# Kernel optimization log

Hardware: AMD Instinct MI355X
Metric: run time of the kernel (lower is better)

Reference implementation:

```python
import jax, jax.numpy as jnp
import numpy as np

NHEADS = 16

def setup_inputs() -> dict:
    key = jax.random.key(0)
    ks = jax.random.split(key, 11)
    B, S, D = 2, 2048, 1024
    std = 1.0 / np.sqrt(D)
    return {
        "query": jax.random.normal(ks[0], (B, S, D), jnp.float32),
        "key":   jax.random.normal(ks[1], (B, S, D), jnp.float32),
        "value": jax.random.normal(ks[2], (B, S, D), jnp.float32),
        "Wq": jax.random.normal(ks[3], (D, D), jnp.float32) * std,
        "bq": jax.random.normal(ks[4], (D,), jnp.float32) * std,
        "Wk": jax.random.normal(ks[5], (D, D), jnp.float32) * std,
        "bk": jax.random.normal(ks[6], (D,), jnp.float32) * std,
        "Wv": jax.random.normal(ks[7], (D, D), jnp.float32) * std,
        "bv": jax.random.normal(ks[8], (D,), jnp.float32) * std,
        "Wo": jax.random.normal(ks[9], (D, D), jnp.float32) * std,
        "bo": jax.random.normal(ks[10], (D,), jnp.float32) * std,
    }

def reference(query, key, value, Wq, bq, Wk, bk, Wv, bv, Wo, bo):
    B, Sq, D = query.shape
    Sk = key.shape[1]
    H = NHEADS
    hd = D // H
    q = (query @ Wq + bq).reshape(B, Sq, H, hd)
    k = (key @ Wk + bk).reshape(B, Sk, H, hd)
    v = (value @ Wv + bv).reshape(B, Sk, H, hd)
    # Explicit [B,H,Sq,Sk] score tensor, as in the original
    score = jnp.einsum('bqhd,bkhd->bhqk', q, k)
    # masked=True: causal mask applied before scaling (equivalent: -inf/c = -inf)
    cmask = jnp.triu(jnp.ones((Sq, Sk), dtype=bool), k=1)
    score = jnp.where(cmask, -jnp.inf, score)
    # NOTE: original divides by sqrt(score.shape[-1]) == sqrt(Sk), NOT sqrt(head_dim)
    scale = jnp.float32(1.0 / np.sqrt(Sk))
    att = jax.nn.softmax(score * scale, axis=-1)
    ret = jnp.einsum('bhqk,bkhd->bqhd', att, v).reshape(B, Sq, D)
    return ret @ Wo + bo
```

## Files before the change

### kernel.cpp

```cpp
#include <hip/hip_runtime.h>
#include <stdint.h>

typedef unsigned short u16;
typedef unsigned int u32;
typedef __bf16 bf16x8 __attribute__((ext_vector_type(8)));
typedef __bf16 bf16x4 __attribute__((ext_vector_type(4)));
typedef float f32x4 __attribute__((ext_vector_type(4)));

__device__ __forceinline__ u16 f2bf(float f) {
  u32 u = __float_as_uint(f);
  u = (u + 0x7fffu + ((u >> 16) & 1u)) >> 16;
  return (u16)u;
}

__device__ __forceinline__ void gload16(const void* g, void* l) {
  __builtin_amdgcn_global_load_lds(
      (const __attribute__((address_space(1))) void*)g,
      (__attribute__((address_space(3))) void*)l, 16, 0, 0);
}

__global__ __launch_bounds__(256) void prep_k(
    const float* __restrict__ q, const float* __restrict__ k,
    const float* __restrict__ v, u16* __restrict__ dst,
    const float* __restrict__ w0, const float* __restrict__ w1,
    const float* __restrict__ w2, const float* __restrict__ w3,
    u16* __restrict__ wt) {
  const int id = blockIdx.x;
  if (id < 6144) {
    const int y = id >> 11;
    const int x = id & 2047;
    const float* s = (y == 0) ? q : (y == 1) ? k : v;
    u16* d = dst + (size_t)y * 4194304u;
    int e = (x * 256 + threadIdx.x) * 8;
    float4 a = *(const float4*)(s + e);
    float4 b = *(const float4*)(s + e + 4);
    uint4 o;
    o.x = (u32)f2bf(a.x) | ((u32)f2bf(a.y) << 16);
    o.y = (u32)f2bf(a.z) | ((u32)f2bf(a.w) << 16);
    o.z = (u32)f2bf(b.x) | ((u32)f2bf(b.y) << 16);
    o.w = (u32)f2bf(b.z) | ((u32)f2bf(b.w) << 16);
    *(uint4*)(d + e) = o;
    return;
  }
  __shared__ float tile[64][65];
  const int t = id - 6144;
  const int z = t >> 8;
  const int rem = t & 255;
  const int x0 = (rem & 15) * 64, y0 = (rem >> 4) * 64;
  const float* W = (z == 0) ? w0 : (z == 1) ? w1 : (z == 2) ? w2 : w3;
  u16* Wt = wt + (size_t)z * 1048576u;
  const int tx = threadIdx.x & 63, ty = threadIdx.x >> 6;
#pragma unroll
  for (int j = 0; j < 16; ++j)
    tile[ty + j * 4][tx] = W[(size_t)(y0 + ty + j * 4) * 1024 + x0 + tx];
  __syncthreads();
#pragma unroll
  for (int j = 0; j < 16; ++j)
    Wt[(size_t)(x0 + ty + j * 4) * 1024 + y0 + tx] = f2bf(tile[tx][ty + j * 4]);
}

__global__ __launch_bounds__(256, 3) void gemm_proj(
    const u16* __restrict__ Xb, const u16* __restrict__ Wt,
    const float* __restrict__ bqp, const float* __restrict__ bkp,
    const float* __restrict__ bvp,
    u16* __restrict__ Qb, u16* __restrict__ Kb, u16* __restrict__ VtG,
    float qsc) {
  const int z = blockIdx.z;
  const u16 *A, *Bt;
  const float* bias;
  u16* C;
  int N, bm, bn;
  float osc = 1.f;
  bool rowb = false;
  if (z < 2) {
    A = Xb + (size_t)z * 4194304u;
    Bt = Wt + (size_t)z * 1048576u;
    bias = z ? bkp : bqp;
    C = z ? Kb : Qb;
    N = 1024;
    bm = blockIdx.x * 128;
    bn = blockIdx.y * 128;
    if (z == 0) osc = qsc;
  } else {
    A = Wt + 2u * 1048576u;
    Bt = Xb + 2u * 4194304u;
    bias = bvp;
    C = VtG;
    N = 4096;
    bm = blockIdx.y * 128;
    bn = blockIdx.x * 128;
    rowb = true;
  }

  __shared__ __align__(16) u16 ldsA[128 * 64];
  __shared__ __align__(16) u16 ldsB[128 * 64];

  const int tid = threadIdx.x;
  const int lane = tid & 63, wv = tid >> 6;
  const int wr = wv >> 1, wc = wv & 1;
  const int l15 = lane & 15, l4 = lane >> 4;

  const f32x4 zero4 = {0.f, 0.f, 0.f, 0.f};
  f32x4 acc[4][4];
#pragma unroll
  for (int i = 0; i < 4; ++i)
#pragma unroll
    for (int j = 0; j < 4; ++j) acc[i][j] = zero4;

  for (int kt = 0; kt < 16; ++kt) {
    __syncthreads();
#pragma unroll
    for (int g = 0; g < 4; ++g) {
      int p = g * 256 + tid;
      int row = p >> 3;
      int ss = (p & 7) ^ (row & 7);
      gload16(A + (size_t)(bm + row) * 1024 + kt * 64 + ss * 8,
              (char*)ldsA + (g * 256 + wv * 64) * 16);
    }
#pragma unroll
    for (int g = 0; g < 4; ++g) {
      int p = g * 256 + tid;
      int row = p >> 3;
      int ss = (p & 7) ^ (row & 7);
      gload16(Bt + (size_t)(bn + row) * 1024 + kt * 64 + ss * 8,
              (char*)ldsB + (g * 256 + wv * 64) * 16);
    }
    __syncthreads();

    bf16x8 af[4][2], bfr[4][2];
#pragma unroll
    for (int mf = 0; mf < 4; ++mf) {
      int row = wr * 64 + mf * 16 + l15;
#pragma unroll
      for (int ks = 0; ks < 2; ++ks) {
        int byt = row * 128 + ((ks * 64 + l4 * 16) ^ ((row & 7) << 4));
        af[mf][ks] = *(const bf16x8*)((const char*)ldsA + byt);
      }
    }
#pragma unroll
    for (int nf = 0; nf < 4; ++nf) {
      int row = wc * 64 + nf * 16 + l15;
#pragma unroll
      for (int ks = 0; ks < 2; ++ks) {
        int byt = row * 128 + ((ks * 64 + l4 * 16) ^ ((row & 7) << 4));
        bfr[nf][ks] = *(const bf16x8*)((const char*)ldsB + byt);
      }
    }
#pragma unroll
    for (int mf = 0; mf < 4; ++mf)
#pragma unroll
      for (int nf = 0; nf < 4; ++nf) {
        acc[mf][nf] = __builtin_amdgcn_mfma_f32_16x16x32_bf16(
            af[mf][0], bfr[nf][0], acc[mf][nf], 0, 0, 0);
        acc[mf][nf] = __builtin_amdgcn_mfma_f32_16x16x32_bf16(
            af[mf][1], bfr[nf][1], acc[mf][nf], 0, 0, 0);
      }
  }

  float bcol[4];
  if (!rowb) {
#pragma unroll
    for (int nf = 0; nf < 4; ++nf)
      bcol[nf] = bias[bn + wc * 64 + nf * 16 + l15];
  }
#pragma unroll
  for (int mf = 0; mf < 4; ++mf) {
#pragma unroll
    for (int i = 0; i < 4; ++i) {
      int r = bm + wr * 64 + mf * 16 + l4 * 4 + i;
      float br = rowb ? bias[r] : 0.f;
#pragma unroll
      for (int nf = 0; nf < 4; ++nf) {
        int c = bn + wc * 64 + nf * 16 + l15;
        float val = (acc[mf][nf][i] + (rowb ? br : bcol[nf])) * osc;
        C[(size_t)r * N + c] = f2bf(val);
      }
    }
  }
}

__global__ __launch_bounds__(256, 3) void gemm_out(
    const u16* __restrict__ A, const u16* __restrict__ Bt,
    const float* __restrict__ bias, float* __restrict__ C) {
  __shared__ __align__(16) u16 ldsA[128 * 64];
  __shared__ __align__(16) u16 ldsB[128 * 64];

  const int tid = threadIdx.x;
  const int lane = tid & 63, wv = tid >> 6;
  const int wr = wv >> 1, wc = wv & 1;
  const int l15 = lane & 15, l4 = lane >> 4;
  const int bm = blockIdx.x * 128, bn = blockIdx.y * 128;

  const f32x4 zero4 = {0.f, 0.f, 0.f, 0.f};
  f32x4 acc[4][4];
#pragma unroll
  for (int i = 0; i < 4; ++i)
#pragma unroll
    for (int j = 0; j < 4; ++j) acc[i][j] = zero4;

  for (int kt = 0; kt < 16; ++kt) {
    __syncthreads();
#pragma unroll
    for (int g = 0; g < 4; ++g) {
      int p = g * 256 + tid;
      int row = p >> 3;
      int ss = (p & 7) ^ (row & 7);
      gload16(A + (size_t)(bm + row) * 1024 + kt * 64 + ss * 8,
              (char*)ldsA + (g * 256 + wv * 64) * 16);
    }
#pragma unroll
    for (int g = 0; g < 4; ++g) {
      int p = g * 256 + tid;
      int row = p >> 3;
      int ss = (p & 7) ^ (row & 7);
      gload16(Bt + (size_t)(bn + row) * 1024 + kt * 64 + ss * 8,
              (char*)ldsB + (g * 256 + wv * 64) * 16);
    }
    __syncthreads();

    bf16x8 af[4][2], bfr[4][2];
#pragma unroll
    for (int mf = 0; mf < 4; ++mf) {
      int row = wr * 64 + mf * 16 + l15;
#pragma unroll
      for (int ks = 0; ks < 2; ++ks) {
        int byt = row * 128 + ((ks * 64 + l4 * 16) ^ ((row & 7) << 4));
        af[mf][ks] = *(const bf16x8*)((const char*)ldsA + byt);
      }
    }
#pragma unroll
    for (int nf = 0; nf < 4; ++nf) {
      int row = wc * 64 + nf * 16 + l15;
#pragma unroll
      for (int ks = 0; ks < 2; ++ks) {
        int byt = row * 128 + ((ks * 64 + l4 * 16) ^ ((row & 7) << 4));
        bfr[nf][ks] = *(const bf16x8*)((const char*)ldsB + byt);
      }
    }
#pragma unroll
    for (int mf = 0; mf < 4; ++mf)
#pragma unroll
      for (int nf = 0; nf < 4; ++nf) {
        acc[mf][nf] = __builtin_amdgcn_mfma_f32_16x16x32_bf16(
            af[mf][0], bfr[nf][0], acc[mf][nf], 0, 0, 0);
        acc[mf][nf] = __builtin_amdgcn_mfma_f32_16x16x32_bf16(
            af[mf][1], bfr[nf][1], acc[mf][nf], 0, 0, 0);
      }
  }

  float bcol[4];
#pragma unroll
  for (int nf = 0; nf < 4; ++nf)
    bcol[nf] = bias[bn + wc * 64 + nf * 16 + l15];
#pragma unroll
  for (int mf = 0; mf < 4; ++mf) {
#pragma unroll
    for (int i = 0; i < 4; ++i) {
      int r = bm + wr * 64 + mf * 16 + l4 * 4 + i;
#pragma unroll
      for (int nf = 0; nf < 4; ++nf) {
        int c = bn + wc * 64 + nf * 16 + l15;
        C[(size_t)r * 1024 + c] = acc[mf][nf][i] + bcol[nf];
      }
    }
  }
}

__global__ __launch_bounds__(256, 2) void attn_k(
    const u16* __restrict__ Q, const u16* __restrict__ Kb,
    const u16* __restrict__ Vt, u16* __restrict__ ctx) {
  const int id = blockIdx.x + (blockIdx.y << 4);
  const int xcd = id & 7;
  const int kk = id >> 3;
  const int bh = xcd * 4 + (kk & 3);
  const int qtA = kk >> 2;
  const int qtB = 31 - qtA;
  const int b = bh >> 4, h = bh & 15;
  const int tid = threadIdx.x;
  const int lane = tid & 63, wv = tid >> 6;
  const int l15 = lane & 15, l4 = lane >> 4;

  __shared__ __align__(16) u16 Kt[2][64 * 64];
  __shared__ __align__(16) u16 Vl[2][64 * 64];
  __shared__ __align__(16) u16 Pl[4][16 * 64];

  const u16* KB = Kb + (size_t)(b * 2048) * 1024 + h * 64;
  const u16* VB = Vt + (size_t)(h * 64) * 4096 + b * 2048;

  const u16* qpa =
      Q + (size_t)(b * 2048 + qtA * 64 + wv * 16 + l15) * 1024 + h * 64;
  const u16* qpb =
      Q + (size_t)(b * 2048 + qtB * 64 + wv * 16 + l15) * 1024 + h * 64;
  bf16x8 qa0 = *(const bf16x8*)(qpa + l4 * 8);
  bf16x8 qa1 = *(const bf16x8*)(qpa + 32 + l4 * 8);
  bf16x8 qb0 = *(const bf16x8*)(qpb + l4 * 8);
  bf16x8 qb1 = *(const bf16x8*)(qpb + 32 + l4 * 8);

  const f32x4 zero4 = {0.f, 0.f, 0.f, 0.f};
  f32x4 oA[4], oB[4];
#pragma unroll
  for (int i = 0; i < 4; ++i) { oA[i] = zero4; oB[i] = zero4; }
  float mA = -1e30f, lsA = 0.f, mB = -1e30f, lsB = 0.f;

  auto issueKV = [&](int jt, int bufi) {
    const u16* kb = KB + (size_t)(jt * 64) * 1024;
#pragma unroll
    for (int g = 0; g < 2; ++g) {
      int p = g * 256 + tid;
      int row = p >> 3;
      int ss = (p & 7) ^ (row & 7);
      gload16(kb + (size_t)row * 1024 + ss * 8,
              (char*)(&Kt[bufi][0]) + (g * 256 + wv * 64) * 16);
    }
#pragma unroll
    for (int g = 0; g < 2; ++g) {
      int p = g * 256 + tid;
      int d = p >> 3;
      int ss = (p & 7) ^ (d & 7);
      gload16(VB + (size_t)d * 4096 + jt * 64 + ss * 8,
              (char*)(&Vl[bufi][0]) + (g * 256 + wv * 64) * 16);
    }
  };

  auto computeTile = [&](int cur, bool diag, bf16x8 qf0, bf16x8 qf1,
                         float& m, float& lsum, f32x4* oacc) {
    f32x4 p4[4];
    __builtin_amdgcn_s_setprio(1);
#pragma unroll
    for (int nt = 0; nt < 4; ++nt) {
      int row = nt * 16 + l15;
      int sw = (row & 7) << 4;
      const char* kr = (const char*)&Kt[cur][0] + row * 128;
      bf16x8 k0 = *(const bf16x8*)(kr + ((l4 * 16) ^ sw));
      bf16x8 k1 = *(const bf16x8*)(kr + ((64 + l4 * 16) ^ sw));
      f32x4 s = zero4;
      s = __builtin_amdgcn_mfma_f32_16x16x32_bf16(k0, qf0, s, 0, 0, 0);
      s = __builtin_amdgcn_mfma_f32_16x16x32_bf16(k1, qf1, s, 0, 0, 0);
      p4[nt] = s;
    }
    __builtin_amdgcn_s_setprio(0);

    if (diag) {
#pragma unroll
      for (int nt = 0; nt < 4; ++nt)
#pragma unroll
        for (int i = 0; i < 4; ++i)
          if (nt * 16 + l4 * 4 + i > wv * 16 + l15) p4[nt][i] = -1e30f;
    }

    float rm = p4[0][0];
#pragma unroll
    for (int nt = 0; nt < 4; ++nt)
#pragma unroll
      for (int i = 0; i < 4; ++i) rm = fmaxf(rm, p4[nt][i]);
    rm = fmaxf(rm, __shfl_xor(rm, 16, 64));
    rm = fmaxf(rm, __shfl_xor(rm, 32, 64));

    if (!__all(rm - m <= 8.0f)) {
      float mn = fmaxf(m, rm);
      float ce = exp2f(m - mn);
      m = mn;
      lsum *= ce;
#pragma unroll
      for (int i = 0; i < 4; ++i) {
        float cei = __shfl(ce, (lane & 48) | (l4 * 4 + i), 64);
#pragma unroll
        for (int nt = 0; nt < 4; ++nt) oacc[nt][i] *= cei;
      }
    }

    float rs = 0.f;
#pragma unroll
    for (int nt = 0; nt < 4; ++nt)
#pragma unroll
      for (int i = 0; i < 4; ++i) {
        float e = exp2f(p4[nt][i] - m);
        p4[nt][i] = e;
        rs += e;
      }
    rs += __shfl_xor(rs, 16, 64);
    rs += __shfl_xor(rs, 32, 64);
    lsum += rs;

    {
      int sw = (l15 & 7) << 4;
#pragma unroll
      for (int nt = 0; nt < 4; ++nt) {
        bf16x4 pb = __builtin_convertvector(p4[nt], bf16x4);
        *(bf16x4*)((char*)&Pl[wv][0] + l15 * 128 + ((nt * 32 + l4 * 8) ^ sw)) = pb;
      }
    }

    bf16x8 pa0, pa1;
    {
      int sw = (l15 & 7) << 4;
      pa0 = *(const bf16x8*)((const char*)&Pl[wv][0] + l15 * 128 + ((l4 * 16) ^ sw));
      pa1 = *(const bf16x8*)((const char*)&Pl[wv][0] + l15 * 128 +
                             ((64 + l4 * 16) ^ sw));
    }
    __builtin_amdgcn_s_setprio(1);
#pragma unroll
    for (int nt = 0; nt < 4; ++nt) {
      int d = nt * 16 + l15;
      int sw = (d & 7) << 4;
      const char* vr = (const char*)&Vl[cur][0] + d * 128;
      bf16x8 v0 = *(const bf16x8*)(vr + ((l4 * 16) ^ sw));
      bf16x8 v1 = *(const bf16x8*)(vr + ((64 + l4 * 16) ^ sw));
      oacc[nt] = __builtin_amdgcn_mfma_f32_16x16x32_bf16(pa0, v0, oacc[nt], 0, 0, 0);
      oacc[nt] = __builtin_amdgcn_mfma_f32_16x16x32_bf16(pa1, v1, oacc[nt], 0, 0, 0);
    }
    __builtin_amdgcn_s_setprio(0);
  };

  issueKV(0, 0);
  for (int j = 0; j <= qtB; ++j) {
    const int cur = j & 1;
    __syncthreads();
    if (j < qtB) issueKV(j + 1, cur ^ 1);
    computeTile(cur, j == qtB, qb0, qb1, mB, lsB, oB);
    if (j <= qtA) computeTile(cur, j == qtA, qa0, qa1, mA, lsA, oA);
  }

  float rcpA = 1.f / lsA;
  float rcpB = 1.f / lsB;
  u16* ca = ctx + (size_t)(b * 2048 + qtA * 64 + wv * 16) * 1024 + h * 64;
  u16* cb = ctx + (size_t)(b * 2048 + qtB * 64 + wv * 16) * 1024 + h * 64;
#pragma unroll
  for (int i = 0; i < 4; ++i) {
    int src = (lane & 48) | (l4 * 4 + i);
    float ivA = __shfl(rcpA, src, 64);
    float ivB = __shfl(rcpB, src, 64);
    int r = l4 * 4 + i;
#pragma unroll
    for (int nt = 0; nt < 4; ++nt) {
      ca[(size_t)r * 1024 + nt * 16 + l15] = f2bf(oA[nt][i] * ivA);
      cb[(size_t)r * 1024 + nt * 16 + l15] = f2bf(oB[nt][i] * ivB);
    }
  }
}

extern "C" void kernel_launch(void* const* d_in, const int* in_sizes, int n_in,
                              void* d_out, int out_size, void* d_ws,
                              size_t ws_size, hipStream_t stream) {
  const float* q  = (const float*)d_in[0];
  const float* k  = (const float*)d_in[1];
  const float* v  = (const float*)d_in[2];
  const float* Wq = (const float*)d_in[3];
  const float* bq = (const float*)d_in[4];
  const float* Wk = (const float*)d_in[5];
  const float* bk = (const float*)d_in[6];
  const float* Wv = (const float*)d_in[7];
  const float* bv = (const float*)d_in[8];
  const float* Wo = (const float*)d_in[9];
  const float* bo = (const float*)d_in[10];

  char* ws = (char*)d_ws;
  u16* Xb  = (u16*)ws;
  u16* Wt  = (u16*)(ws + 25165824);
  u16* VtG = (u16*)(ws + 33554432);
  u16* ctx = Xb;
  u16* Qb  = (u16*)d_out;
  u16* Kb  = Qb + 4194304;

  const float SC2A = 0.0318793585f;

  prep_k<<<dim3(7168), 256, 0, stream>>>(q, k, v, Xb, Wq, Wk, Wv, Wo, Wt);
  gemm_proj<<<dim3(32, 8, 3), 256, 0, stream>>>(Xb, Wt, bq, bk, bv, Qb, Kb,
                                                VtG, SC2A);
  attn_k<<<dim3(16, 32), 256, 0, stream>>>(Qb, Kb, VtG, ctx);
  gemm_out<<<dim3(32, 8), 256, 0, stream>>>(ctx, Wt + 3 * 1048576, bo,
                                            (float*)d_out);
}
```

Measured before the change: 114.4 us.

## Fuse fp32-to-bf16 activation conversion into projection GEMM staging

Removes the separate pass that converts q/k/v activations to bf16. The projection GEMM now reads fp32 activations directly, converts them in registers and writes them into LDS, while weights still use async global-to-LDS loads. This saves the write and re-read of a 24MB bf16 intermediate. In exchange, each GEMM tile reads fp32 data (twice the bytes, re-read across N tiles) through registers instead of direct LDS loads, and the MFMA block is also given a raised scheduling priority.

```diff
diff --git a/kernel.cpp b/kernel.cpp
--- a/kernel.cpp
+++ b/kernel.cpp
@@ -20,30 +20,11 @@
 }
 
 __global__ __launch_bounds__(256) void prep_k(
-    const float* __restrict__ q, const float* __restrict__ k,
-    const float* __restrict__ v, u16* __restrict__ dst,
     const float* __restrict__ w0, const float* __restrict__ w1,
     const float* __restrict__ w2, const float* __restrict__ w3,
     u16* __restrict__ wt) {
-  const int id = blockIdx.x;
-  if (id < 6144) {
-    const int y = id >> 11;
-    const int x = id & 2047;
-    const float* s = (y == 0) ? q : (y == 1) ? k : v;
-    u16* d = dst + (size_t)y * 4194304u;
-    int e = (x * 256 + threadIdx.x) * 8;
-    float4 a = *(const float4*)(s + e);
-    float4 b = *(const float4*)(s + e + 4);
-    uint4 o;
-    o.x = (u32)f2bf(a.x) | ((u32)f2bf(a.y) << 16);
-    o.y = (u32)f2bf(a.z) | ((u32)f2bf(a.w) << 16);
-    o.z = (u32)f2bf(b.x) | ((u32)f2bf(b.y) << 16);
-    o.w = (u32)f2bf(b.z) | ((u32)f2bf(b.w) << 16);
-    *(uint4*)(d + e) = o;
-    return;
-  }
   __shared__ float tile[64][65];
-  const int t = id - 6144;
+  const int t = blockIdx.x;
   const int z = t >> 8;
   const int rem = t & 255;
   const int x0 = (rem & 15) * 64, y0 = (rem >> 4) * 64;
@@ -60,21 +41,23 @@
 }
 
 __global__ __launch_bounds__(256, 3) void gemm_proj(
-    const u16* __restrict__ Xb, const u16* __restrict__ Wt,
+    const float* __restrict__ qin, const float* __restrict__ kin,
+    const float* __restrict__ vin, const u16* __restrict__ Wt,
     const float* __restrict__ bqp, const float* __restrict__ bkp,
     const float* __restrict__ bvp,
     u16* __restrict__ Qb, u16* __restrict__ Kb, u16* __restrict__ VtG,
     float qsc) {
   const int z = blockIdx.z;
-  const u16 *A, *Bt;
+  const float* Xf;
+  const u16* Wb;
   const float* bias;
   u16* C;
   int N, bm, bn;
   float osc = 1.f;
   bool rowb = false;
   if (z < 2) {
-    A = Xb + (size_t)z * 4194304u;
-    Bt = Wt + (size_t)z * 1048576u;
+    Xf = z ? kin : qin;
+    Wb = Wt + (size_t)z * 1048576u;
     bias = z ? bkp : bqp;
     C = z ? Kb : Qb;
     N = 1024;
@@ -82,8 +65,8 @@
     bn = blockIdx.y * 128;
     if (z == 0) osc = qsc;
   } else {
-    A = Wt + 2u * 1048576u;
-    Bt = Xb + 2u * 4194304u;
+    Wb = Wt + 2u * 1048576u;
+    Xf = vin;
     bias = bvp;
     C = VtG;
     N = 4096;
@@ -107,23 +90,42 @@
 #pragma unroll
     for (int j = 0; j < 4; ++j) acc[i][j] = zero4;
 
+  auto stageF32 = [&](const float* S, int baseRow, int kt, u16* lds) {
+#pragma unroll
+    for (int g = 0; g < 4; ++g) {
+      int p = g * 256 + tid;
+      int row = p >> 3;
+      int ss = (p & 7) ^ (row & 7);
+      const float* src = S + (size_t)(baseRow + row) * 1024 + kt * 64 + ss * 8;
+      float4 a = *(const float4*)(src);
+      float4 b = *(const float4*)(src + 4);
+      uint4 o;
+      o.x = (u32)f2bf(a.x) | ((u32)f2bf(a.y) << 16);
+      o.y = (u32)f2bf(a.z) | ((u32)f2bf(a.w) << 16);
+      o.z = (u32)f2bf(b.x) | ((u32)f2bf(b.y) << 16);
+      o.w = (u32)f2bf(b.z) | ((u32)f2bf(b.w) << 16);
+      *(uint4*)((char*)lds + (size_t)(g * 256 + tid) * 16) = o;
+    }
+  };
+  auto stageBf = [&](const u16* S, int baseRow, int kt, u16* lds) {
+#pragma unroll
+    for (int g = 0; g < 4; ++g) {
+      int p = g * 256 + tid;
+      int row = p >> 3;
+      int ss = (p & 7) ^ (row & 7);
+      gload16(S + (size_t)(baseRow + row) * 1024 + kt * 64 + ss * 8,
+              (char*)lds + (size_t)(g * 256 + wv * 64) * 16);
+    }
+  };
+
   for (int kt = 0; kt < 16; ++kt) {
     __syncthreads();
-#pragma unroll
-    for (int g = 0; g < 4; ++g) {
-      int p = g * 256 + tid;
-      int row = p >> 3;
-      int ss = (p & 7) ^ (row & 7);
-      gload16(A + (size_t)(bm + row) * 1024 + kt * 64 + ss * 8,
-              (char*)ldsA + (g * 256 + wv * 64) * 16);
-    }
-#pragma unroll
-    for (int g = 0; g < 4; ++g) {
-      int p = g * 256 + tid;
-      int row = p >> 3;
-      int ss = (p & 7) ^ (row & 7);
-      gload16(Bt + (size_t)(bn + row) * 1024 + kt * 64 + ss * 8,
-              (char*)ldsB + (g * 256 + wv * 64) * 16);
+    if (z < 2) {
+      stageF32(Xf, bm, kt, ldsA);
+      stageBf(Wb, bn, kt, ldsB);
+    } else {
+      stageBf(Wb, bm, kt, ldsA);
+      stageF32(Xf, bn, kt, ldsB);
     }
     __syncthreads();
 
@@ -146,6 +148,7 @@
         bfr[nf][ks] = *(const bf16x8*)((const char*)ldsB + byt);
       }
     }
+    __builtin_amdgcn_s_setprio(1);
 #pragma unroll
     for (int mf = 0; mf < 4; ++mf)
 #pragma unroll
@@ -155,6 +158,7 @@
         acc[mf][nf] = __builtin_amdgcn_mfma_f32_16x16x32_bf16(
             af[mf][1], bfr[nf][1], acc[mf][nf], 0, 0, 0);
       }
+    __builtin_amdgcn_s_setprio(0);
   }
 
   float bcol[4];
@@ -455,18 +459,17 @@
   const float* bo = (const float*)d_in[10];
 
   char* ws = (char*)d_ws;
-  u16* Xb  = (u16*)ws;
+  u16* ctx = (u16*)ws;
   u16* Wt  = (u16*)(ws + 25165824);
   u16* VtG = (u16*)(ws + 33554432);
-  u16* ctx = Xb;
   u16* Qb  = (u16*)d_out;
   u16* Kb  = Qb + 4194304;
 
   const float SC2A = 0.0318793585f;
 
-  prep_k<<<dim3(7168), 256, 0, stream>>>(q, k, v, Xb, Wq, Wk, Wv, Wo, Wt);
-  gemm_proj<<<dim3(32, 8, 3), 256, 0, stream>>>(Xb, Wt, bq, bk, bv, Qb, Kb,
-                                                VtG, SC2A);
+  prep_k<<<dim3(1024), 256, 0, stream>>>(Wq, Wk, Wv, Wo, Wt);
+  gemm_proj<<<dim3(32, 8, 3), 256, 0, stream>>>(q, k, v, Wt, bq, bk, bv,
+                                                Qb, Kb, VtG, SC2A);
   attn_k<<<dim3(16, 32), 256, 0, stream>>>(Qb, Kb, VtG, ctx);
   gemm_out<<<dim3(32, 8), 256, 0, stream>>>(ctx, Wt + 3 * 1048576, bo,
                                             (float*)d_out);
```

New measurement: 132.0 us. 15.4% more time.

## Fuse paired query tiles into one pass sharing K/V fragment loads

Applied to the files above, without the earlier changes.

While both query tiles A and B are active, the loop computes their scores and PV products together. Each K and V fragment is read from LDS once and used for both tiles, and the independent MFMA chains are interleaved to hide latency. When A is on its diagonal tile, B still needs the full tile, so B is left unmasked, which matches the old behaviour. The P scratch buffer doubles in size to hold both tiles, and register pressure rises, which may hurt the occupancy of 2 blocks per CU.

```diff
diff --git a/kernel.cpp b/kernel.cpp
--- a/kernel.cpp
+++ b/kernel.cpp
@@ -282,7 +282,7 @@
 
   __shared__ __align__(16) u16 Kt[2][64 * 64];
   __shared__ __align__(16) u16 Vl[2][64 * 64];
-  __shared__ __align__(16) u16 Pl[4][16 * 64];
+  __shared__ __align__(16) u16 Pl[4][32 * 64];
 
   const u16* KB = Kb + (size_t)(b * 2048) * 1024 + h * 64;
   const u16* VB = Vt + (size_t)(h * 64) * 4096 + b * 2048;
@@ -320,6 +320,40 @@
       gload16(VB + (size_t)d * 4096 + jt * 64 + ss * 8,
               (char*)(&Vl[bufi][0]) + (g * 256 + wv * 64) * 16);
     }
+  };
+
+  auto softmaxUpd = [&](f32x4* p4, float& m, float& ls, f32x4* oacc) {
+    float rm = p4[0][0];
+#pragma unroll
+    for (int nt = 0; nt < 4; ++nt)
+#pragma unroll
+      for (int i = 0; i < 4; ++i) rm = fmaxf(rm, p4[nt][i]);
+    rm = fmaxf(rm, __shfl_xor(rm, 16, 64));
+    rm = fmaxf(rm, __shfl_xor(rm, 32, 64));
+    if (!__all(rm - m <= 8.0f)) {
+      float mn = fmaxf(m, rm);
+      float ce = exp2f(m - mn);
+      m = mn;
+      ls *= ce;
+#pragma unroll
+      for (int i = 0; i < 4; ++i) {
+        float cei = __shfl(ce, (lane & 48) | (l4 * 4 + i), 64);
+#pragma unroll
+        for (int nt = 0; nt < 4; ++nt) oacc[nt][i] *= cei;
+      }
+    }
+    float rs = 0.f;
+#pragma unroll
+    for (int nt = 0; nt < 4; ++nt)
+#pragma unroll
+      for (int i = 0; i < 4; ++i) {
+        float e = exp2f(p4[nt][i] - m);
+        p4[nt][i] = e;
+        rs += e;
+      }
+    rs += __shfl_xor(rs, 16, 64);
+    rs += __shfl_xor(rs, 32, 64);
+    ls += rs;
   };
 
   auto computeTile = [&](int cur, bool diag, bf16x8 qf0, bf16x8 qf1,
@@ -339,7 +373,6 @@
       p4[nt] = s;
     }
     __builtin_amdgcn_s_setprio(0);
-
     if (diag) {
 #pragma unroll
       for (int nt = 0; nt < 4; ++nt)
@@ -347,65 +380,25 @@
         for (int i = 0; i < 4; ++i)
           if (nt * 16 + l4 * 4 + i > wv * 16 + l15) p4[nt][i] = -1e30f;
     }
-
-    float rm = p4[0][0];
-#pragma unroll
-    for (int nt = 0; nt < 4; ++nt)
-#pragma unroll
-      for (int i = 0; i < 4; ++i) rm = fmaxf(rm, p4[nt][i]);
-    rm = fmaxf(rm, __shfl_xor(rm, 16, 64));
-    rm = fmaxf(rm, __shfl_xor(rm, 32, 64));
-
-    if (!__all(rm - m <= 8.0f)) {
-      float mn = fmaxf(m, rm);
-      float ce = exp2f(m - mn);
-      m = mn;
-      lsum *= ce;
-#pragma unroll
-      for (int i = 0; i < 4; ++i) {
-        float cei = __shfl(ce, (lane & 48) | (l4 * 4 + i), 64);
-#pragma unroll
-        for (int nt = 0; nt < 4; ++nt) oacc[nt][i] *= cei;
-      }
-    }
-
-    float rs = 0.f;
-#pragma unroll
-    for (int nt = 0; nt < 4; ++nt)
-#pragma unroll
-      for (int i = 0; i < 4; ++i) {
-        float e = exp2f(p4[nt][i] - m);
-        p4[nt][i] = e;
-        rs += e;
-      }
-    rs += __shfl_xor(rs, 16, 64);
-    rs += __shfl_xor(rs, 32, 64);
-    lsum += rs;
-
-    {
-      int sw = (l15 & 7) << 4;
-#pragma unroll
-      for (int nt = 0; nt < 4; ++nt) {
-        bf16x4 pb = __builtin_convertvector(p4[nt], bf16x4);
-        *(bf16x4*)((char*)&Pl[wv][0] + l15 * 128 + ((nt * 32 + l4 * 8) ^ sw)) = pb;
-      }
-    }
-
-    bf16x8 pa0, pa1;
-    {
-      int sw = (l15 & 7) << 4;
-      pa0 = *(const bf16x8*)((const char*)&Pl[wv][0] + l15 * 128 + ((l4 * 16) ^ sw));
-      pa1 = *(const bf16x8*)((const char*)&Pl[wv][0] + l15 * 128 +
-                             ((64 + l4 * 16) ^ sw));
-    }
+    softmaxUpd(p4, m, lsum, oacc);
+    const int sw = (l15 & 7) << 4;
+#pragma unroll
+    for (int nt = 0; nt < 4; ++nt) {
+      bf16x4 pb = __builtin_convertvector(p4[nt], bf16x4);
+      *(bf16x4*)((char*)&Pl[wv][0] + l15 * 128 + ((nt * 32 + l4 * 8) ^ sw)) = pb;
+    }
+    bf16x8 pa0 =
+        *(const bf16x8*)((const char*)&Pl[wv][0] + l15 * 128 + ((l4 * 16) ^ sw));
+    bf16x8 pa1 = *(const bf16x8*)((const char*)&Pl[wv][0] + l15 * 128 +
+                                  ((64 + l4 * 16) ^ sw));
     __builtin_amdgcn_s_setprio(1);
 #pragma unroll
     for (int nt = 0; nt < 4; ++nt) {
       int d = nt * 16 + l15;
-      int sw = (d & 7) << 4;
+      int sw2 = (d & 7) << 4;
       const char* vr = (const char*)&Vl[cur][0] + d * 128;
-      bf16x8 v0 = *(const bf16x8*)(vr + ((l4 * 16) ^ sw));
-      bf16x8 v1 = *(const bf16x8*)(vr + ((64 + l4 * 16) ^ sw));
+      bf16x8 v0 = *(const bf16x8*)(vr + ((l4 * 16) ^ sw2));
+      bf16x8 v1 = *(const bf16x8*)(vr + ((64 + l4 * 16) ^ sw2));
       oacc[nt] = __builtin_amdgcn_mfma_f32_16x16x32_bf16(pa0, v0, oacc[nt], 0, 0, 0);
       oacc[nt] = __builtin_amdgcn_mfma_f32_16x16x32_bf16(pa1, v1, oacc[nt], 0, 0, 0);
     }
@@ -417,8 +410,69 @@
     const int cur = j & 1;
     __syncthreads();
     if (j < qtB) issueKV(j + 1, cur ^ 1);
-    computeTile(cur, j == qtB, qb0, qb1, mB, lsB, oB);
-    if (j <= qtA) computeTile(cur, j == qtA, qa0, qa1, mA, lsA, oA);
+
+    if (j <= qtA) {
+      f32x4 pA[4], pB[4];
+      __builtin_amdgcn_s_setprio(1);
+#pragma unroll
+      for (int nt = 0; nt < 4; ++nt) {
+        int row = nt * 16 + l15;
+        int sw = (row & 7) << 4;
+        const char* kr = (const char*)&Kt[cur][0] + row * 128;
+        bf16x8 k0 = *(const bf16x8*)(kr + ((l4 * 16) ^ sw));
+        bf16x8 k1 = *(const bf16x8*)(kr + ((64 + l4 * 16) ^ sw));
+        f32x4 sA = __builtin_amdgcn_mfma_f32_16x16x32_bf16(k0, qa0, zero4, 0, 0, 0);
+        f32x4 sB = __builtin_amdgcn_mfma_f32_16x16x32_bf16(k0, qb0, zero4, 0, 0, 0);
+        sA = __builtin_amdgcn_mfma_f32_16x16x32_bf16(k1, qa1, sA, 0, 0, 0);
+        sB = __builtin_amdgcn_mfma_f32_16x16x32_bf16(k1, qb1, sB, 0, 0, 0);
+        pA[nt] = sA;
+        pB[nt] = sB;
+      }
+      __builtin_amdgcn_s_setprio(0);
+
+      if (j == qtA) {
+#pragma unroll
+        for (int nt = 0; nt < 4; ++nt)
+#pragma unroll
+          for (int i = 0; i < 4; ++i)
+            if (nt * 16 + l4 * 4 + i > wv * 16 + l15) pA[nt][i] = -1e30f;
+      }
+
+      softmaxUpd(pA, mA, lsA, oA);
+      softmaxUpd(pB, mB, lsB, oB);
+
+      const int sw = (l15 & 7) << 4;
+      char* prA = (char*)&Pl[wv][0] + l15 * 128;
+      char* prB = (char*)&Pl[wv][0] + (16 + l15) * 128;
+#pragma unroll
+      for (int nt = 0; nt < 4; ++nt) {
+        *(bf16x4*)(prA + ((nt * 32 + l4 * 8) ^ sw)) =
+            __builtin_convertvector(pA[nt], bf16x4);
+        *(bf16x4*)(prB + ((nt * 32 + l4 * 8) ^ sw)) =
+            __builtin_convertvector(pB[nt], bf16x4);
+      }
+      bf16x8 paA0 = *(const bf16x8*)(prA + ((l4 * 16) ^ sw));
+      bf16x8 paA1 = *(const bf16x8*)(prA + ((64 + l4 * 16) ^ sw));
+      bf16x8 paB0 = *(const bf16x8*)(prB + ((l4 * 16) ^ sw));
+      bf16x8 paB1 = *(const bf16x8*)(prB + ((64 + l4 * 16) ^ sw));
+
+      __builtin_amdgcn_s_setprio(1);
+#pragma unroll
+      for (int nt = 0; nt < 4; ++nt) {
+        int d = nt * 16 + l15;
+        int sw2 = (d & 7) << 4;
+        const char* vr = (const char*)&Vl[cur][0] + d * 128;
+        bf16x8 v0 = *(const bf16x8*)(vr + ((l4 * 16) ^ sw2));
+        bf16x8 v1 = *(const bf16x8*)(vr + ((64 + l4 * 16) ^ sw2));
+        oA[nt] = __builtin_amdgcn_mfma_f32_16x16x32_bf16(paA0, v0, oA[nt], 0, 0, 0);
+        oB[nt] = __builtin_amdgcn_mfma_f32_16x16x32_bf16(paB0, v0, oB[nt], 0, 0, 0);
+        oA[nt] = __builtin_amdgcn_mfma_f32_16x16x32_bf16(paA1, v1, oA[nt], 0, 0, 0);
+        oB[nt] = __builtin_amdgcn_mfma_f32_16x16x32_bf16(paB1, v1, oB[nt], 0, 0, 0);
+      }
+      __builtin_amdgcn_s_setprio(0);
+    } else {
+      computeTile(cur, j == qtB, qb0, qb1, mB, lsB, oB);
+    }
   }
 
   float rcpA = 1.f / lsA;
```

Measured after the change: 116.0 us. No clear change (+1.4%).
